# Kernel optimization log

Measured on AMD Instinct MI355X. Metric: run time of the kernel, lower is better.

The kernel has to match this reference:

```python
import jax, jax.numpy as jnp
import numpy as np

B, T, D = 4, 2048, 512
H, HS = 8, 64            # n_head, head_size
E, K = 8, 2              # num_experts, top_k
CAP = int(B * T * K / E * 1.0)  # expert capacity = 2048
EPS = 1e-5


def setup_inputs() -> dict:
    key = jax.random.key(0)
    ks = jax.random.split(key, 16)
    s = lambda k, shp, fan: jax.random.normal(k, shp, jnp.float32) * (fan ** -0.5)
    return {
        "x": jax.random.normal(ks[0], (B, T, D), jnp.float32),
        "ln1_g": jnp.ones((D,), jnp.float32), "ln1_b": jnp.zeros((D,), jnp.float32),
        "Wq": s(ks[1], (H, D, HS), D), "Wk": s(ks[2], (H, D, HS), D), "Wv": s(ks[3], (H, D, HS), D),
        "Wo": s(ks[4], (D, D), D), "bo": jnp.zeros((D,), jnp.float32),
        "ln2_g": jnp.ones((D,), jnp.float32), "ln2_b": jnp.zeros((D,), jnp.float32),
        "Wg": s(ks[5], (D, E), D), "bg": jnp.zeros((E,), jnp.float32),
        "Wn": s(ks[6], (D, E), D), "bn": jnp.zeros((E,), jnp.float32),
        "W1": s(ks[7], (E, D, 4 * D), D), "b1": jnp.zeros((E, 4 * D), jnp.float32),
        "W2": s(ks[8], (E, 4 * D, D), 4 * D), "b2": jnp.zeros((E, D), jnp.float32),
    }


def _ln(x, g, b):
    m = jnp.mean(x, -1, keepdims=True)
    v = jnp.var(x, -1, keepdims=True)
    return (x - m) * jax.lax.rsqrt(v + EPS) * g + b


def _attn(h, Wq, Wk, Wv, Wo, bo):
    q = jnp.einsum('btd,hde->bhte', h, Wq)
    k = jnp.einsum('btd,hde->bhte', h, Wk)
    v = jnp.einsum('btd,hde->bhte', h, Wv)
    # NOTE: source scales by C**-0.5 with C = n_embed (not head_size)
    wei = jnp.einsum('bhte,bhse->bhts', q, k) * (D ** -0.5)
    causal = jnp.tril(jnp.ones((T, T), bool))
    wei = jnp.where(causal, wei, -jnp.inf)
    wei = jax.nn.softmax(wei, axis=-1)
    out = jnp.einsum('bhts,bhse->bhte', wei, v)              # [B,H,T,HS]
    out = out.transpose(0, 2, 1, 3).reshape(B, T, D)          # concat heads
    return out @ Wo + bo


def _moe(h, Wg, bg, Wn, bn, W1, b1, W2, b2):
    logits = h @ Wg + bg
    noise_logits = h @ Wn + bn
    noise = jax.random.normal(jax.random.key(42), logits.shape, logits.dtype) * jax.nn.softplus(noise_logits)
    noisy = logits + noise
    vals, idx = jax.lax.top_k(noisy, K)                       # [B,T,K]
    # softmax over -inf-masked sparse logits == softmax over top-k values, scattered
    gates = (jax.nn.softmax(vals, -1)[..., None] * jax.nn.one_hot(idx, E, dtype=h.dtype)).sum(-2)  # [B,T,E]
    flat_x = h.reshape(-1, D)
    flat_g = gates.reshape(-1, E)
    flat_idx = idx.reshape(-1, K)
    N = flat_x.shape[0]
    mask = (flat_idx[None] == jnp.arange(E)[:, None, None]).any(-1)   # [E,N]
    rank = jnp.cumsum(mask, axis=1) - 1
    keep = mask & (rank < CAP)                                 # first CAP tokens per expert
    slot = jnp.where(keep, rank, CAP)
    tok = jnp.arange(N, dtype=jnp.int32)

    def build(s, kp):
        buf = jnp.zeros(CAP + 1, jnp.int32).at[s].set(tok)
        vb = jnp.zeros(CAP + 1, bool).at[s].set(kp)
        return buf[:CAP], vb[:CAP]

    idx_buf, valid = jax.vmap(build)(slot, keep)               # [E,CAP]
    xg = flat_x[idx_buf]                                       # [E,CAP,D]
    mid = jax.nn.relu(jnp.einsum('ecd,edf->ecf', xg, W1) + b1[:, None, :])
    out = jnp.einsum('ecf,efd->ecd', mid, W2) + b2[:, None, :]
    gate_sel = flat_g[idx_buf, jnp.arange(E)[:, None]]         # [E,CAP]
    w = out * (gate_sel * valid.astype(h.dtype))[..., None]
    upd = jnp.zeros_like(flat_x).at[idx_buf.reshape(-1)].add(w.reshape(-1, D))
    return upd.reshape(h.shape)


def reference(x, ln1_g, ln1_b, Wq, Wk, Wv, Wo, bo, ln2_g, ln2_b,
              Wg, bg, Wn, bn, W1, b1, W2, b2):
    x = x + _attn(_ln(x, ln1_g, ln1_b), Wq, Wk, Wv, Wo, bo)
    x = x + _moe(_ln(x, ln2_g, ln2_b), Wg, bg, Wn, bn, W1, b1, W2, b2)
    return x
```

## Files before the change

kernel.cpp:

```cpp
#include <hip/hip_runtime.h>
#include <math.h>

#define TSEQ 2048
#define DD   512
#define NH   8
#define HSZ  64
#define NE   8
#define NTOK 8192
#define CAPK 2048
#define FF   2048

typedef __bf16 bf16x8 __attribute__((ext_vector_type(8)));
typedef float  f32x4  __attribute__((ext_vector_type(4)));
typedef unsigned int u32;
typedef u32 u32x4 __attribute__((ext_vector_type(4)));

__device__ __forceinline__ void gload16(const void* g, void* l){
  __builtin_amdgcn_global_load_lds((const __attribute__((address_space(1))) u32*)g,
                                   (__attribute__((address_space(3))) u32*)l, 16, 0, 0);
}

__device__ __forceinline__ u32 pkbf(float a, float b){
  unsigned short ua = __builtin_bit_cast(unsigned short, (__bf16)a);
  unsigned short ub = __builtin_bit_cast(unsigned short, (__bf16)b);
  return (u32)ua | ((u32)ub << 16);
}

__device__ __forceinline__ unsigned rotl32(unsigned x, int r){ return (x<<r)|(x>>(32-r)); }

__device__ __forceinline__ void threefry2x32(unsigned c0, unsigned c1, unsigned &o0, unsigned &o1){
  const unsigned k0 = 0u, k1 = 42u;
  const unsigned k2 = k0 ^ k1 ^ 0x1BD11BDAu;
  unsigned x0 = c0 + k0, x1 = c1 + k1;
#define TFR(rot) { x0 += x1; x1 = rotl32(x1, rot); x1 ^= x0; }
  TFR(13) TFR(15) TFR(26) TFR(6)   x0 += k1; x1 += k2 + 1u;
  TFR(17) TFR(29) TFR(16) TFR(24)  x0 += k2; x1 += k0 + 2u;
  TFR(13) TFR(15) TFR(26) TFR(6)   x0 += k0; x1 += k1 + 3u;
  TFR(17) TFR(29) TFR(16) TFR(24)  x0 += k1; x1 += k2 + 4u;
  TFR(13) TFR(15) TFR(26) TFR(6)   x0 += k2; x1 += k0 + 5u;
#undef TFR
  o0 = x0; o1 = x1;
}

__device__ __forceinline__ float erfinv_f(float x){
  float w = -log1pf(-x*x);
  float p;
  if (w < 5.0f){
    w -= 2.5f;
    p = 2.81022636e-08f;
    p = fmaf(p,w, 3.43273939e-07f);
    p = fmaf(p,w,-3.5233877e-06f);
    p = fmaf(p,w,-4.39150654e-06f);
    p = fmaf(p,w, 0.00021858087f);
    p = fmaf(p,w,-0.00125372503f);
    p = fmaf(p,w,-0.00417768164f);
    p = fmaf(p,w, 0.246640727f);
    p = fmaf(p,w, 1.50140941f);
  } else {
    w = sqrtf(w) - 3.0f;
    p = -0.000200214257f;
    p = fmaf(p,w, 0.000100950558f);
    p = fmaf(p,w, 0.00134934322f);
    p = fmaf(p,w,-0.00367342844f);
    p = fmaf(p,w, 0.00573950773f);
    p = fmaf(p,w,-0.0076224613f);
    p = fmaf(p,w, 0.00943887047f);
    p = fmaf(p,w, 1.00167406f);
    p = fmaf(p,w, 2.83297682f);
  }
  return p * x;
}

__global__ __launch_bounds__(256) void ln_split(const float* __restrict__ x,
    const float* __restrict__ gw, const float* __restrict__ bw,
    __bf16* __restrict__ ohi, __bf16* __restrict__ olo)
{
  int row  = blockIdx.x*4 + threadIdx.y;
  int lane = threadIdx.x;
  const float* xr = x + (size_t)row*DD;
  float4 a = *(const float4*)(xr + lane*4);
  float4 c = *(const float4*)(xr + 256 + lane*4);
  float s  = a.x+a.y+a.z+a.w + c.x+c.y+c.z+c.w;
  float ss = a.x*a.x+a.y*a.y+a.z*a.z+a.w*a.w + c.x*c.x+c.y*c.y+c.z*c.z+c.w*c.w;
  #pragma unroll
  for (int off = 32; off; off >>= 1){ s += __shfl_xor(s, off); ss += __shfl_xor(ss, off); }
  float m   = s * (1.0f/DD);
  float var = ss * (1.0f/DD) - m*m;
  float r   = 1.0f / sqrtf(var + 1e-5f);
  float4 g1 = *(const float4*)(gw + lane*4);
  float4 b1 = *(const float4*)(bw + lane*4);
  float4 g2 = *(const float4*)(gw + 256 + lane*4);
  float4 b2 = *(const float4*)(bw + 256 + lane*4);
  float f1[4], f2[4];
  f1[0]=(a.x-m)*r*g1.x+b1.x; f1[1]=(a.y-m)*r*g1.y+b1.y; f1[2]=(a.z-m)*r*g1.z+b1.z; f1[3]=(a.w-m)*r*g1.w+b1.w;
  f2[0]=(c.x-m)*r*g2.x+b2.x; f2[1]=(c.y-m)*r*g2.y+b2.y; f2[2]=(c.z-m)*r*g2.z+b2.z; f2[3]=(c.w-m)*r*g2.w+b2.w;
  __bf16 h1v[4] __attribute__((aligned(8))), l1v[4] __attribute__((aligned(8)));
  __bf16 h2v[4] __attribute__((aligned(8))), l2v[4] __attribute__((aligned(8)));
  #pragma unroll
  for (int j = 0; j < 4; ++j){
    __bf16 hb = (__bf16)f1[j]; h1v[j]=hb; l1v[j]=(__bf16)(f1[j]-(float)hb);
    __bf16 hc = (__bf16)f2[j]; h2v[j]=hc; l2v[j]=(__bf16)(f2[j]-(float)hc);
  }
  size_t base = (size_t)row*DD + lane*4;
  *(uint2*)(ohi + base)       = *(const uint2*)h1v;
  *(uint2*)(olo + base)       = *(const uint2*)l1v;
  *(uint2*)(ohi + base + 256) = *(const uint2*)h2v;
  *(uint2*)(olo + base + 256) = *(const uint2*)l2v;
}

__global__ __launch_bounds__(256) void pack_qkv_split(const float* __restrict__ Wq,
    const float* __restrict__ Wk, const float* __restrict__ Wv,
    __bf16* __restrict__ dhi, __bf16* __restrict__ dlo)
{
  __shared__ float t[64][65];
  int z = blockIdx.y;
  int kt = blockIdx.x*64;
  int sel = z >> 3, hh = z & 7;
  const float* W = (sel==0 ? Wq : (sel==1 ? Wk : Wv)) + (size_t)hh*DD*HSZ;
  int tid = threadIdx.x;
  int r = tid>>2, c0 = (tid&3)*16;
  #pragma unroll
  for (int j = 0; j < 16; j += 4){
    float4 v = *(const float4*)&W[(size_t)(kt+r)*HSZ + c0 + j];
    t[r][c0+j]=v.x; t[r][c0+j+1]=v.y; t[r][c0+j+2]=v.z; t[r][c0+j+3]=v.w;
  }
  __syncthreads();
  __bf16 hb[16] __attribute__((aligned(32)));
  __bf16 lb[16] __attribute__((aligned(32)));
  #pragma unroll
  for (int j = 0; j < 16; ++j){
    float f = t[c0+j][r];
    __bf16 h = (__bf16)f; hb[j]=h; lb[j]=(__bf16)(f-(float)h);
  }
  size_t off = (size_t)(z*64 + r)*512 + kt + c0;
  *(uint4*)(dhi+off) = ((const uint4*)hb)[0]; *(uint4*)(dhi+off+8) = ((const uint4*)hb)[1];
  *(uint4*)(dlo+off) = ((const uint4*)lb)[0]; *(uint4*)(dlo+off+8) = ((const uint4*)lb)[1];
}

__global__ __launch_bounds__(256) void transp_split(const float* __restrict__ src,
    __bf16* __restrict__ dhi, __bf16* __restrict__ dlo, int Ms, int Ns)
{
  __shared__ float t[64][65];
  int nt = blockIdx.x*64, mt = blockIdx.y*64;
  int tid = threadIdx.x;
  int r = tid>>2, c0 = (tid&3)*16;
  #pragma unroll
  for (int j = 0; j < 16; j += 4){
    float4 v = *(const float4*)&src[(size_t)(mt+r)*Ns + nt + c0 + j];
    t[r][c0+j]=v.x; t[r][c0+j+1]=v.y; t[r][c0+j+2]=v.z; t[r][c0+j+3]=v.w;
  }
  __syncthreads();
  __bf16 hb[16] __attribute__((aligned(32)));
  __bf16 lb[16] __attribute__((aligned(32)));
  #pragma unroll
  for (int j = 0; j < 16; ++j){
    float f = t[c0+j][r];
    __bf16 h = (__bf16)f; hb[j]=h; lb[j]=(__bf16)(f-(float)h);
  }
  size_t off = (size_t)(nt + r)*Ms + mt + c0;
  *(uint4*)(dhi+off) = ((const uint4*)hb)[0]; *(uint4*)(dhi+off+8) = ((const uint4*)hb)[1];
  *(uint4*)(dlo+off) = ((const uint4*)lb)[0]; *(uint4*)(dlo+off+8) = ((const uint4*)lb)[1];
}

template<int BIAS, int RES>
__global__ __launch_bounds__(256) void gemm_mfma3(
    const __bf16* __restrict__ Ahi, const __bf16* __restrict__ Alo,
    const __bf16* __restrict__ Bhi, const __bf16* __restrict__ Blo,
    const float* __restrict__ bias, const float* __restrict__ res,
    float* __restrict__ C, int M, int N, int K)
{
  __shared__ __bf16 AsH[2][4096];
  __shared__ __bf16 AsL[2][4096];
  __shared__ __bf16 BsH[2][4096];
  __shared__ __bf16 BsL[2][4096];
  int m0 = blockIdx.y*128, n0 = blockIdx.x*128;
  int tid = threadIdx.x;
  int w = tid>>6, l = tid&63;
  int wm = w>>1, wn = w&1;
  int srow = w*32 + (l>>2);
  int skb  = (l&3)<<4;
  const char* agh = (const char*)(Ahi + (size_t)(m0+srow)*K) + skb;
  const char* agl = (const char*)(Alo + (size_t)(m0+srow)*K) + skb;
  const char* bgh = (const char*)(Bhi + (size_t)(n0+srow)*K) + skb;
  const char* bgl = (const char*)(Blo + (size_t)(n0+srow)*K) + skb;
  size_t r16 = (size_t)16*K*sizeof(__bf16);

  f32x4 acc[4][4] = {};
  int rl = l & 15, kh = l >> 4;
  const __bf16* abh = &AsH[0][(wm*64 + rl)*32 + kh*8];
  const __bf16* abl = &AsL[0][(wm*64 + rl)*32 + kh*8];
  const __bf16* bbh = &BsH[0][(wn*64 + rl)*32 + kh*8];
  const __bf16* bbl = &BsL[0][(wn*64 + rl)*32 + kh*8];

  auto STAGE = [&](int bb, int kt){
    size_t o = (size_t)kt*64;
    gload16(agh+o,     &AsH[bb][w*1024]);
    gload16(agh+o+r16, &AsH[bb][w*1024+512]);
    gload16(agl+o,     &AsL[bb][w*1024]);
    gload16(agl+o+r16, &AsL[bb][w*1024+512]);
    gload16(bgh+o,     &BsH[bb][w*1024]);
    gload16(bgh+o+r16, &BsH[bb][w*1024+512]);
    gload16(bgl+o,     &BsL[bb][w*1024]);
    gload16(bgl+o+r16, &BsL[bb][w*1024+512]);
  };

  int nkt = K >> 5;
  STAGE(0, 0);
  __syncthreads();
  for (int kt = 0; kt < nkt; ++kt){
    int bb = kt & 1;
    if (kt + 1 < nkt) STAGE(bb^1, kt+1);
    bf16x8 afh[4], afl[4], bfh[4], bfl[4];
    #pragma unroll
    for (int i = 0; i < 4; ++i){
      afh[i] = *(const bf16x8*)(abh + bb*4096 + i*512);
      afl[i] = *(const bf16x8*)(abl + bb*4096 + i*512);
      bfh[i] = *(const bf16x8*)(bbh + bb*4096 + i*512);
      bfl[i] = *(const bf16x8*)(bbl + bb*4096 + i*512);
    }
    #pragma unroll
    for (int fm = 0; fm < 4; ++fm)
      #pragma unroll
      for (int fn = 0; fn < 4; ++fn){
        acc[fm][fn] = __builtin_amdgcn_mfma_f32_16x16x32_bf16(afh[fm], bfl[fn], acc[fm][fn], 0, 0, 0);
        acc[fm][fn] = __builtin_amdgcn_mfma_f32_16x16x32_bf16(afl[fm], bfh[fn], acc[fm][fn], 0, 0, 0);
        acc[fm][fn] = __builtin_amdgcn_mfma_f32_16x16x32_bf16(afh[fm], bfh[fn], acc[fm][fn], 0, 0, 0);
      }
    __syncthreads();
  }

  int ccol = l & 15, cr = (l >> 4) * 4;
  #pragma unroll
  for (int fn = 0; fn < 4; ++fn){
    int n = n0 + wn*64 + fn*16 + ccol;
    float bv = BIAS ? bias[n] : 0.0f;
    #pragma unroll
    for (int fm = 0; fm < 4; ++fm){
      int mb = m0 + wm*64 + fm*16 + cr;
      #pragma unroll
      for (int r = 0; r < 4; ++r){
        float v = acc[fm][fn][r] + bv;
        if (RES) v += res[(size_t)(mb+r)*N + n];
        C[(size_t)(mb+r)*N + n] = v;
      }
    }
  }
}

template<int STORE_BF16, int RELU, int GATHER, int LOGN>
__global__ __launch_bounds__(256) void gemm_mfma(
    const __bf16* __restrict__ A, const __bf16* __restrict__ Bt,
    const float* __restrict__ bias, void* __restrict__ Cv,
    const int* __restrict__ idxb, int M, int N, int K)
{
  __shared__ __bf16 Asl[2][4096];
  __shared__ __bf16 Bsl[2][4096];
  int flat = blockIdx.x;
  int e = flat & 3;
  int tile = flat >> 2;
  int n0 = (tile & ((1<<LOGN)-1)) * 128;
  int m0 = (tile >> LOGN) * 128;
  const __bf16* Be = Bt + (size_t)e*N*K;
  const float*  be = bias + (size_t)e*N;
  int tid = threadIdx.x;
  int w = tid>>6, l = tid&63;
  int wm = w>>1, wn = w&1;
  int srow = w*32 + (l>>2);
  int skb  = (l&3)<<4;
  const char* ag;
  if (GATHER){
    int tok = idxb[e*CAPK + m0 + srow];
    ag = (const char*)(A + (size_t)tok*K) + skb;
  } else {
    ag = (const char*)(A + (size_t)e*M*K + (size_t)(m0 + srow)*K) + skb;
  }
  const char* bg = (const char*)(Be + (size_t)(n0 + srow)*K) + skb;
  size_t r16;
  if (GATHER){
    int tok2 = idxb[e*CAPK + m0 + srow + 16];
    r16 = (size_t)((const char*)(A + (size_t)tok2*K) + skb - ag);
  } else {
    r16 = (size_t)16*K*sizeof(__bf16);
  }

  f32x4 acc[4][4] = {};
  int rl = l & 15, kh = l >> 4;
  const __bf16* abase = &Asl[0][(wm*64 + rl)*32 + kh*8];
  const __bf16* bbase = &Bsl[0][(wn*64 + rl)*32 + kh*8];

  size_t br16 = (size_t)16*K*sizeof(__bf16);
  auto STAGE = [&](int bb, int kt){
    size_t o = (size_t)kt*64;
    gload16(ag+o,      &Asl[bb][w*1024]);
    gload16(ag+o+r16,  &Asl[bb][w*1024+512]);
    gload16(bg+o,      &Bsl[bb][w*1024]);
    gload16(bg+o+br16, &Bsl[bb][w*1024+512]);
  };

  int nkt = K >> 5;
  STAGE(0, 0);
  __syncthreads();
  for (int kt = 0; kt < nkt; ++kt){
    int bb = kt & 1;
    if (kt + 1 < nkt) STAGE(bb^1, kt+1);
    bf16x8 af[4], bf[4];
    #pragma unroll
    for (int i = 0; i < 4; ++i){
      af[i] = *(const bf16x8*)(abase + bb*4096 + i*512);
      bf[i] = *(const bf16x8*)(bbase + bb*4096 + i*512);
    }
    #pragma unroll
    for (int fm = 0; fm < 4; ++fm)
      #pragma unroll
      for (int fn = 0; fn < 4; ++fn)
        acc[fm][fn] = __builtin_amdgcn_mfma_f32_16x16x32_bf16(af[fm], bf[fn], acc[fm][fn], 0, 0, 0);
    __syncthreads();
  }

  int ccol = l & 15, cr = (l >> 4) * 4;
  char* Ce = (char*)Cv + (size_t)e*M*N*(STORE_BF16 ? 2 : 4);
  #pragma unroll
  for (int fn = 0; fn < 4; ++fn){
    int n = n0 + wn*64 + fn*16 + ccol;
    float bv = be[n];
    #pragma unroll
    for (int fm = 0; fm < 4; ++fm){
      int mb = m0 + wm*64 + fm*16 + cr;
      #pragma unroll
      for (int r = 0; r < 4; ++r){
        float v = acc[fm][fn][r] + bv;
        if (RELU) v = fmaxf(v, 0.f);
        if (STORE_BF16) ((__bf16*)Ce)[(size_t)(mb+r)*N + n] = (__bf16)v;
        else            ((float*)Ce)[(size_t)(mb+r)*N + n] = v;
      }
    }
  }
}

__global__ __launch_bounds__(256) void transp_conv(const float* __restrict__ src,
    __bf16* __restrict__ dst, int Ms, int Ns)
{
  __shared__ __bf16 t[64][72];
  int e = blockIdx.z;
  const float* s = src + (size_t)e*Ms*Ns;
  __bf16* d = dst + (size_t)e*Ms*Ns;
  int mt = blockIdx.y*64, nt = blockIdx.x*64;
  int tid = threadIdx.x;
  int r = tid>>2, c0 = (tid&3)*16;
  #pragma unroll
  for (int j = 0; j < 16; j += 4){
    float4 v = *(const float4*)&s[(size_t)(mt+r)*Ns + nt + c0 + j];
    t[r][c0+j]   = (__bf16)v.x; t[r][c0+j+1] = (__bf16)v.y;
    t[r][c0+j+2] = (__bf16)v.z; t[r][c0+j+3] = (__bf16)v.w;
  }
  __syncthreads();
  __bf16 tmp[16] __attribute__((aligned(32)));
  #pragma unroll
  for (int j = 0; j < 16; ++j) tmp[j] = t[c0+j][r];
  uint4* dp = (uint4*)&d[(size_t)(nt+r)*Ms + mt + c0];
  dp[0] = ((const uint4*)tmp)[0];
  dp[1] = ((const uint4*)tmp)[1];
}

__global__ __launch_bounds__(256) void convert_kv(const float* __restrict__ qkv,
    __bf16* __restrict__ khi, __bf16* __restrict__ klo,
    __bf16* __restrict__ vthi, __bf16* __restrict__ vtlo)
{
  int t0 = blockIdx.x*64;
  int bh = blockIdx.y;
  int b = bh >> 3, h = bh & 7;
  int tid = threadIdx.x;
  {
    int r = tid >> 2, e0 = (tid & 3) * 16;
    const float* src = qkv + ((size_t)(b*TSEQ + t0 + r))*1536 + 512 + h*64 + e0;
    __bf16 hi[16] __attribute__((aligned(16)));
    __bf16 lo[16] __attribute__((aligned(16)));
    #pragma unroll
    for (int j = 0; j < 16; j += 4){
      float4 v = *(const float4*)(src + j);
      float f[4] = {v.x, v.y, v.z, v.w};
      #pragma unroll
      for (int q = 0; q < 4; ++q){
        __bf16 hb = (__bf16)f[q];
        hi[j+q] = hb; lo[j+q] = (__bf16)(f[q] - (float)hb);
      }
    }
    size_t off = ((size_t)(bh*TSEQ + t0 + r))*64 + e0;
    *(uint4*)(khi + off)     = ((const uint4*)hi)[0];
    *(uint4*)(khi + off + 8) = ((const uint4*)hi)[1];
    *(uint4*)(klo + off)     = ((const uint4*)lo)[0];
    *(uint4*)(klo + off + 8) = ((const uint4*)lo)[1];
  }
  {
    int key0 = (tid & 15) * 4, e0 = (tid >> 4) * 4;
    float4 v[4];
    #pragma unroll
    for (int j = 0; j < 4; ++j)
      v[j] = *(const float4*)(qkv + ((size_t)(b*TSEQ + t0 + key0 + j))*1536 + 1024 + h*64 + e0);
    float col[4][4];
    col[0][0]=v[0].x; col[0][1]=v[1].x; col[0][2]=v[2].x; col[0][3]=v[3].x;
    col[1][0]=v[0].y; col[1][1]=v[1].y; col[1][2]=v[2].y; col[1][3]=v[3].y;
    col[2][0]=v[0].z; col[2][1]=v[1].z; col[2][2]=v[2].z; col[2][3]=v[3].z;
    col[3][0]=v[0].w; col[3][1]=v[1].w; col[3][2]=v[2].w; col[3][3]=v[3].w;
    #pragma unroll
    for (int kk = 0; kk < 4; ++kk){
      __bf16 hi[4] __attribute__((aligned(8)));
      __bf16 lo[4] __attribute__((aligned(8)));
      #pragma unroll
      for (int j = 0; j < 4; ++j){
        __bf16 hb = (__bf16)col[kk][j];
        hi[j] = hb; lo[j] = (__bf16)(col[kk][j] - (float)hb);
      }
      size_t off = ((size_t)(bh*64 + e0 + kk))*TSEQ + t0 + key0;
      *(uint2*)(vthi + off) = *(const uint2*)hi;
      *(uint2*)(vtlo + off) = *(const uint2*)lo;
    }
  }
}

__global__ __launch_bounds__(512) void attn_mfma(const float* __restrict__ qkv,
    const __bf16* __restrict__ khi_g, const __bf16* __restrict__ klo_g,
    const __bf16* __restrict__ vthi_g, const __bf16* __restrict__ vtlo_g,
    __bf16* __restrict__ ahi, __bf16* __restrict__ alo)
{
  __shared__ __align__(16) char ldsbuf[65536];
  int bh = blockIdx.x;
  int qtA = blockIdx.y, qtB = 15 - qtA;
  int b = bh >> 3, h = bh & 7;
  int tid = threadIdx.x;
  int w = tid >> 6, l = tid & 63;
  int g = l >> 4, r = l & 15;
  int sA = r + 32*(g & 1);
  int sB = sA + 16;
  int ghalf = g >> 1;
  const float qsc = 0.04419417382415922f * 1.4426950408889634f;

  int qb[2]; qb[0] = qtA*128 + w*16; qb[1] = qtB*128 + (7-w)*16;
  int kdiag[2]; kdiag[0] = qb[0] >> 6; kdiag[1] = qb[1] >> 6;

  bf16x8 qhi[2][2], qlo[2][2];
  #pragma unroll
  for (int qf = 0; qf < 2; ++qf)
    #pragma unroll
    for (int ks = 0; ks < 2; ++ks){
      const float* src = qkv + ((size_t)(b*TSEQ + qb[qf] + r))*1536 + h*64 + ks*32 + g*8;
      float4 v0 = *(const float4*)src;
      float4 v1 = *(const float4*)(src + 4);
      float f[8] = {v0.x,v0.y,v0.z,v0.w,v1.x,v1.y,v1.z,v1.w};
      bf16x8 hi, lo;
      #pragma unroll
      for (int i = 0; i < 8; ++i){
        float fs = f[i] * qsc;
        __bf16 hb = (__bf16)fs;
        hi[i] = hb; lo[i] = (__bf16)(fs - (float)hb);
      }
      qhi[qf][ks] = hi; qlo[qf][ks] = lo;
    }

  f32x4 ot[4][2] = {};
  float m_r[2] = {-INFINITY, -INFINITY};
  float l_r[2] = {0.f, 0.f};

  int nkt = 2*qtB + 2;
  size_t kbase = (size_t)bh*TSEQ*64;
  size_t vbase = (size_t)bh*64*TSEQ;

  auto STAGE = [&](int buf, int kt){
    int row = tid >> 3, cc = tid & 7;
    int sw = (cc ^ (row & 7)) * 8;
    char* d = ldsbuf + buf*32768 + (w << 10);
    gload16(khi_g  + kbase + (size_t)(kt*64 + row)*64 + sw, d);
    gload16(klo_g  + kbase + (size_t)(kt*64 + row)*64 + sw, d + 8192);
    gload16(vthi_g + vbase + (size_t)row*TSEQ + kt*64 + sw,  d + 16384);
    gload16(vtlo_g + vbase + (size_t)row*TSEQ + kt*64 + sw,  d + 24576);
  };

  STAGE(0, 0);
  __syncthreads();

  for (int kt = 0; kt < nkt; ++kt){
    int buf = kt & 1;
    if (kt + 1 < nkt) STAGE(buf ^ 1, kt + 1);

    bool act[2];
    act[0] = (kt <= kdiag[0]);
    act[1] = (kt <= kdiag[1]);

    const char* K0 = ldsbuf + buf*32768;
    const char* K1 = K0 + 8192;
    const char* V0 = K0 + 16384;
    const char* V1 = K0 + 24576;

    f32x4 s[4][2] = {};
    #pragma unroll
    for (int kf = 0; kf < 4; ++kf){
      int rowk = kf*16 + r;
      int rsw = (rowk & 7) << 4;
      #pragma unroll
      for (int ks = 0; ks < 2; ++ks){
        int off = rowk*128 + ((((ks*4 + g) << 4)) ^ rsw);
        bf16x8 khf = *(const bf16x8*)(K0 + off);
        bf16x8 klf = *(const bf16x8*)(K1 + off);
        #pragma unroll
        for (int qf = 0; qf < 2; ++qf){
          if (act[qf]){
            s[kf][qf] = __builtin_amdgcn_mfma_f32_16x16x32_bf16(khf, qlo[qf][ks], s[kf][qf], 0,0,0);
            s[kf][qf] = __builtin_amdgcn_mfma_f32_16x16x32_bf16(klf, qhi[qf][ks], s[kf][qf], 0,0,0);
            s[kf][qf] = __builtin_amdgcn_mfma_f32_16x16x32_bf16(khf, qhi[qf][ks], s[kf][qf], 0,0,0);
          }
        }
      }
    }

    u32 phi[4][2][2], plo[4][2][2];
    #pragma unroll
    for (int qf = 0; qf < 2; ++qf){
      if (act[qf]){
        int q = qb[qf] + r;
        float p[4][4];
        float mx = -INFINITY;
        if (kt == kdiag[qf]){
          #pragma unroll
          for (int kf = 0; kf < 4; ++kf)
            #pragma unroll
            for (int e = 0; e < 4; ++e){
              int key = kt*64 + kf*16 + g*4 + e;
              float sv = (key <= q) ? s[kf][qf][e] : -INFINITY;
              p[kf][e] = sv;
              mx = fmaxf(mx, sv);
            }
        } else {
          #pragma unroll
          for (int kf = 0; kf < 4; ++kf)
            #pragma unroll
            for (int e = 0; e < 4; ++e){
              float sv = s[kf][qf][e];
              p[kf][e] = sv;
              mx = fmaxf(mx, sv);
            }
        }
        mx = fmaxf(mx, __shfl_xor(mx, 16));
        mx = fmaxf(mx, __shfl_xor(mx, 32));
        if (__any(mx > m_r[qf])){
          float mn = fmaxf(m_r[qf], mx);
          float fj = exp2f(m_r[qf] - mn);
          m_r[qf] = mn;
          l_r[qf] *= fj;
          #pragma unroll
          for (int ef = 0; ef < 4; ++ef)
            #pragma unroll
            for (int e = 0; e < 4; ++e)
              ot[ef][qf][e] *= fj;
        }
        float ts = 0.f;
        #pragma unroll
        for (int kf = 0; kf < 4; ++kf)
          #pragma unroll
          for (int e = 0; e < 4; ++e){
            float pv = exp2f(p[kf][e] - m_r[qf]);
            p[kf][e] = pv; ts += pv;
          }
        ts += __shfl_xor(ts, 16); ts += __shfl_xor(ts, 32);
        l_r[qf] += ts;
        #pragma unroll
        for (int kf = 0; kf < 4; ++kf){
          __bf16 h0=(__bf16)p[kf][0], h1=(__bf16)p[kf][1], h2=(__bf16)p[kf][2], h3=(__bf16)p[kf][3];
          phi[kf][qf][0] = pkbf(p[kf][0], p[kf][1]);
          phi[kf][qf][1] = pkbf(p[kf][2], p[kf][3]);
          plo[kf][qf][0] = pkbf(p[kf][0]-(float)h0, p[kf][1]-(float)h1);
          plo[kf][qf][1] = pkbf(p[kf][2]-(float)h2, p[kf][3]-(float)h3);
        }
      }
    }

    #pragma unroll
    for (int ks = 0; ks < 2; ++ks){
      u32x4 pbh[2], pbl[2];
      #pragma unroll
      for (int qf = 0; qf < 2; ++qf){
        if (act[qf]){
          #pragma unroll
          for (int p2 = 0; p2 < 2; ++p2){
            u32 hA0 = (u32)__shfl((int)phi[2*ks  ][qf][p2], sA);
            u32 hA1 = (u32)__shfl((int)phi[2*ks+1][qf][p2], sA);
            u32 hB0 = (u32)__shfl((int)phi[2*ks  ][qf][p2], sB);
            u32 hB1 = (u32)__shfl((int)phi[2*ks+1][qf][p2], sB);
            pbh[qf][p2]   = ghalf ? hA1 : hA0;
            pbh[qf][2+p2] = ghalf ? hB1 : hB0;
            u32 lA0 = (u32)__shfl((int)plo[2*ks  ][qf][p2], sA);
            u32 lA1 = (u32)__shfl((int)plo[2*ks+1][qf][p2], sA);
            u32 lB0 = (u32)__shfl((int)plo[2*ks  ][qf][p2], sB);
            u32 lB1 = (u32)__shfl((int)plo[2*ks+1][qf][p2], sB);
            pbl[qf][p2]   = ghalf ? lA1 : lA0;
            pbl[qf][2+p2] = ghalf ? lB1 : lB0;
          }
        }
      }
      #pragma unroll
      for (int ef = 0; ef < 4; ++ef){
        int rowv = ef*16 + r;
        int off = rowv*128 + ((((ks*4 + g) << 4)) ^ ((rowv & 7) << 4));
        bf16x8 vhf = *(const bf16x8*)(V0 + off);
        bf16x8 vlf = *(const bf16x8*)(V1 + off);
        #pragma unroll
        for (int qf = 0; qf < 2; ++qf){
          if (act[qf]){
            bf16x8 ph = __builtin_bit_cast(bf16x8, pbh[qf]);
            bf16x8 pl = __builtin_bit_cast(bf16x8, pbl[qf]);
            ot[ef][qf] = __builtin_amdgcn_mfma_f32_16x16x32_bf16(vhf, pl, ot[ef][qf], 0,0,0);
            ot[ef][qf] = __builtin_amdgcn_mfma_f32_16x16x32_bf16(vlf, ph, ot[ef][qf], 0,0,0);
            ot[ef][qf] = __builtin_amdgcn_mfma_f32_16x16x32_bf16(vhf, ph, ot[ef][qf], 0,0,0);
          }
        }
      }
    }
    __syncthreads();
  }

  float* Osh = (float*)ldsbuf;
  #pragma unroll
  for (int qf = 0; qf < 2; ++qf){
    float inv = 1.0f / l_r[qf];
    int qloc = (qf ? (7-w) : w)*16 + r;
    #pragma unroll
    for (int ef = 0; ef < 4; ++ef)
      #pragma unroll
      for (int e = 0; e < 4; ++e)
        Osh[qloc*68 + ef*16 + g*4 + e] = ot[ef][qf][e] * inv;
    __syncthreads();
    {
      int qt = qf ? qtB : qtA;
      int q = tid >> 2, e0 = (tid & 3)*16;
      const float* srow = Osh + q*68 + e0;
      size_t base = ((size_t)(b*TSEQ + qt*128 + q))*DD + h*64 + e0;
      #pragma unroll
      for (int j = 0; j < 4; ++j){
        float4 v = *(const float4*)(srow + j*4);
        float f[4] = {v.x, v.y, v.z, v.w};
        __bf16 hb[4] __attribute__((aligned(8)));
        __bf16 lb[4] __attribute__((aligned(8)));
        #pragma unroll
        for (int q2 = 0; q2 < 4; ++q2){
          __bf16 h2b = (__bf16)f[q2];
          hb[q2] = h2b; lb[q2] = (__bf16)(f[q2] - (float)h2b);
        }
        *(uint2*)(ahi + base + j*4) = *(const uint2*)hb;
        *(uint2*)(alo + base + j*4) = *(const uint2*)lb;
      }
    }
    __syncthreads();
  }
}

__global__ __launch_bounds__(256) void routerln_kernel(const float* __restrict__ x1,
    const float* __restrict__ gw, const float* __restrict__ bw,
    const float* __restrict__ Wg, const float* __restrict__ bg,
    const float* __restrict__ Wn, const float* __restrict__ bn,
    __bf16* __restrict__ h2b,
    int* __restrict__ idx0, int* __restrict__ idx1,
    float* __restrict__ g0, float* __restrict__ g1)
{
  int wid = threadIdx.x >> 6, lane = threadIdx.x & 63;
  int tok = blockIdx.x*4 + wid;
  const float* xr = x1 + (size_t)tok*DD;
  float4 a = *(const float4*)(xr + lane*4);
  float4 c = *(const float4*)(xr + 256 + lane*4);
  float s  = a.x+a.y+a.z+a.w + c.x+c.y+c.z+c.w;
  float ss = a.x*a.x+a.y*a.y+a.z*a.z+a.w*a.w + c.x*c.x+c.y*c.y+c.z*c.z+c.w*c.w;
  #pragma unroll
  for (int off = 32; off; off >>= 1){ s += __shfl_xor(s, off); ss += __shfl_xor(ss, off); }
  float m   = s * (1.0f/DD);
  float var = ss * (1.0f/DD) - m*m;
  float rr  = 1.0f / sqrtf(var + 1e-5f);
  float4 g1v = *(const float4*)(gw + lane*4);
  float4 b1v = *(const float4*)(bw + lane*4);
  float4 g2v = *(const float4*)(gw + 256 + lane*4);
  float4 b2v = *(const float4*)(bw + 256 + lane*4);
  float f1[4], f2[4];
  f1[0]=(a.x-m)*rr*g1v.x+b1v.x; f1[1]=(a.y-m)*rr*g1v.y+b1v.y; f1[2]=(a.z-m)*rr*g1v.z+b1v.z; f1[3]=(a.w-m)*rr*g1v.w+b1v.w;
  f2[0]=(c.x-m)*rr*g2v.x+b2v.x; f2[1]=(c.y-m)*rr*g2v.y+b2v.y; f2[2]=(c.z-m)*rr*g2v.z+b2v.z; f2[3]=(c.w-m)*rr*g2v.w+b2v.w;
  {
    __bf16 h1v[4] __attribute__((aligned(8)));
    __bf16 h2v[4] __attribute__((aligned(8)));
    #pragma unroll
    for (int j = 0; j < 4; ++j){ h1v[j] = (__bf16)f1[j]; h2v[j] = (__bf16)f2[j]; }
    size_t base = (size_t)tok*DD + lane*4;
    *(uint2*)(h2b + base)       = *(const uint2*)h1v;
    *(uint2*)(h2b + base + 256) = *(const uint2*)h2v;
  }
  float ag[8] = {0,0,0,0,0,0,0,0}, an[8] = {0,0,0,0,0,0,0,0};
  int d1 = lane*4, d2 = 256 + lane*4;
  #pragma unroll
  for (int j = 0; j < 4; ++j){
    const float* wg1 = Wg + (size_t)(d1+j)*8;
    const float* wn1 = Wn + (size_t)(d1+j)*8;
    const float* wg2 = Wg + (size_t)(d2+j)*8;
    const float* wn2 = Wn + (size_t)(d2+j)*8;
    #pragma unroll
    for (int e = 0; e < 8; ++e){
      ag[e] = fmaf(f1[j], wg1[e], ag[e]); an[e] = fmaf(f1[j], wn1[e], an[e]);
      ag[e] = fmaf(f2[j], wg2[e], ag[e]); an[e] = fmaf(f2[j], wn2[e], an[e]);
    }
  }
  #pragma unroll
  for (int off = 32; off; off >>= 1){
    #pragma unroll
    for (int e = 0; e < 8; ++e){ ag[e] += __shfl_xor(ag[e], off); an[e] += __shfl_xor(an[e], off); }
  }
  __shared__ float ns[4][8];
  if (lane < 8){
    int e = lane;
    float lg = ag[e] + bg[e];
    float nl = an[e] + bn[e];
    float sp = fmaxf(nl, 0.f) + log1pf(expf(-fabsf(nl)));
    unsigned i = (unsigned)(tok*8 + e);
    unsigned r0b, r1b;
    threefry2x32(0u, i, r0b, r1b);
    unsigned bits = r0b ^ r1b;
    float f = __uint_as_float((bits >> 9) | 0x3f800000u) - 1.0f;
    float u = fmaf(f, 2.0f, -0.99999994f);
    u = fmaxf(u, -0.99999994f);
    float z = 1.41421356f * erfinv_f(u);
    ns[wid][e] = lg + z*sp;
  }
  __syncthreads();
  if (lane == 0){
    float v0 = -INFINITY; int i0 = 0;
    #pragma unroll
    for (int e = 0; e < 8; ++e){ float v = ns[wid][e]; if (v > v0){ v0 = v; i0 = e; } }
    float v1 = -INFINITY; int i1 = 0;
    #pragma unroll
    for (int e = 0; e < 8; ++e){ if (e != i0){ float v = ns[wid][e]; if (v > v1){ v1 = v; i1 = e; } } }
    float dexp = expf(v1 - v0);
    float ssum = 1.0f + dexp;
    idx0[tok] = i0; idx1[tok] = i1;
    g0[tok] = 1.0f/ssum; g1[tok] = dexp/ssum;
  }
}

__global__ __launch_bounds__(256) void route_scan(const int* __restrict__ idx0,
    const int* __restrict__ idx1, int* __restrict__ idx_buf, int* __restrict__ tok_slot)
{
  int e = blockIdx.x, tid = threadIdx.x;
  for (int i = tid; i < CAPK; i += 256) idx_buf[e*CAPK + i] = 0;
  __syncthreads();
  int base = tid * 32;
  int cnt = 0;
  for (int j = 0; j < 32; ++j){ int t = base + j; cnt += (idx0[t]==e || idx1[t]==e) ? 1 : 0; }
  __shared__ int ps[256];
  ps[tid] = cnt; __syncthreads();
  for (int off = 1; off < 256; off <<= 1){
    int add = (tid >= off) ? ps[tid - off] : 0;
    __syncthreads();
    ps[tid] += add;
    __syncthreads();
  }
  int slot = ps[tid] - cnt;
  for (int j = 0; j < 32; ++j){
    int t = base + j;
    int k = (idx0[t]==e) ? 0 : ((idx1[t]==e) ? 1 : -1);
    if (k >= 0){
      if (slot < CAPK){ idx_buf[e*CAPK + slot] = t; tok_slot[t*2 + k] = slot; }
      else            { tok_slot[t*2 + k] = -1; }
      slot++;
    }
  }
}

__global__ __launch_bounds__(128) void combine_kernel(const float* __restrict__ x1,
    const __bf16* __restrict__ eout, const int* __restrict__ idx0, const int* __restrict__ idx1,
    const float* __restrict__ g0, const float* __restrict__ g1,
    const int* __restrict__ tok_slot, float* __restrict__ outp)
{
  int n = blockIdx.x, t = threadIdx.x;
  float4 acc = *(const float4*)(x1 + (size_t)n*DD + t*4);
  #pragma unroll
  for (int k = 0; k < 2; ++k){
    int s = tok_slot[n*2 + k];
    if (s >= 0){
      int e  = (k==0) ? idx0[n] : idx1[n];
      float g = (k==0) ? g0[n] : g1[n];
      __bf16 vb[4] __attribute__((aligned(8)));
      *(uint2*)vb = *(const uint2*)(eout + ((size_t)(e*CAPK + s))*DD + t*4);
      acc.x = fmaf(g, (float)vb[0], acc.x); acc.y = fmaf(g, (float)vb[1], acc.y);
      acc.z = fmaf(g, (float)vb[2], acc.z); acc.w = fmaf(g, (float)vb[3], acc.w);
    }
  }
  *(float4*)(outp + (size_t)n*DD + t*4) = acc;
}

extern "C" void kernel_launch(void* const* d_in, const int* in_sizes, int n_in,
                              void* d_out, int out_size, void* d_ws, size_t ws_size,
                              hipStream_t stream)
{
  const float* x    = (const float*)d_in[0];
  const float* ln1g = (const float*)d_in[1];
  const float* ln1b = (const float*)d_in[2];
  const float* Wq   = (const float*)d_in[3];
  const float* Wk   = (const float*)d_in[4];
  const float* Wv   = (const float*)d_in[5];
  const float* Wo   = (const float*)d_in[6];
  const float* bo   = (const float*)d_in[7];
  const float* ln2g = (const float*)d_in[8];
  const float* ln2b = (const float*)d_in[9];
  const float* Wg   = (const float*)d_in[10];
  const float* bg   = (const float*)d_in[11];
  const float* Wn   = (const float*)d_in[12];
  const float* bn   = (const float*)d_in[13];
  const float* W1   = (const float*)d_in[14];
  const float* b1   = (const float*)d_in[15];
  const float* W2   = (const float*)d_in[16];
  const float* b2   = (const float*)d_in[17];
  float* out = (float*)d_out;
  char* ws = (char*)d_ws;
  const size_t MB = 1u << 20;

  __bf16* h1hi   = (__bf16*)(ws);
  __bf16* h1lo   = (__bf16*)(ws + 8*MB);
  __bf16* attnhi = (__bf16*)(ws);
  __bf16* attnlo = (__bf16*)(ws + 8*MB);
  __bf16* h2b    = (__bf16*)(ws);
  float*  qkv    = (float*)(ws + 16*MB);
  __bf16* W1T    = (__bf16*)(ws + 16*MB);
  __bf16* W2T    = (__bf16*)(ws + 32*MB);
  float*  x1     = (float*)(ws + 64*MB);
  __bf16* Khi    = (__bf16*)(ws + 80*MB);
  __bf16* Klo    = (__bf16*)(ws + 88*MB);
  __bf16* Vthi   = (__bf16*)(ws + 96*MB);
  __bf16* Vtlo   = (__bf16*)(ws + 104*MB);
  __bf16* Bqh    = (__bf16*)(ws + 80*MB);
  __bf16* Bql    = (__bf16*)(ws + 82*MB);
  __bf16* eoutb  = (__bf16*)(ws + 80*MB);
  __bf16* mid    = (__bf16*)(ws + 112*MB);
  __bf16* WoTh   = (__bf16*)(ws + 144*MB);
  __bf16* WoTl   = (__bf16*)(ws + 144*MB + 512*1024);
  char*   smallp = ws + 145*MB;
  int*   idx0     = (int*)smallp;
  int*   idx1     = idx0 + NTOK;
  float* g0       = (float*)(idx1 + NTOK);
  float* g1       = g0 + NTOK;
  int*   tok_slot = (int*)(g1 + NTOK);
  int*   idx_buf  = tok_slot + NTOK*2;

  ln_split<<<dim3(NTOK/4), dim3(64,4), 0, stream>>>(x, ln1g, ln1b, h1hi, h1lo);
  pack_qkv_split<<<dim3(8,24), 256, 0, stream>>>(Wq, Wk, Wv, Bqh, Bql);
  transp_split<<<dim3(8,8), 256, 0, stream>>>(Wo, WoTh, WoTl, DD, DD);
  gemm_mfma3<0,0><<<dim3(12,64), 256, 0, stream>>>(h1hi, h1lo, Bqh, Bql, nullptr, nullptr, qkv, NTOK, 1536, DD);
  convert_kv<<<dim3(TSEQ/64, 32), 256, 0, stream>>>(qkv, Khi, Klo, Vthi, Vtlo);
  attn_mfma<<<dim3(32, 8), 512, 0, stream>>>(qkv, Khi, Klo, Vthi, Vtlo, attnhi, attnlo);
  gemm_mfma3<1,1><<<dim3(4,64), 256, 0, stream>>>(attnhi, attnlo, WoTh, WoTl, bo, x, x1, NTOK, DD, DD);
  routerln_kernel<<<dim3(NTOK/4), 256, 0, stream>>>(x1, ln2g, ln2b, Wg, bg, Wn, bn,
      h2b, idx0, idx1, g0, g1);
  transp_conv<<<dim3(32,8,NE), 256, 0, stream>>>(W1, W1T, DD, FF);
  transp_conv<<<dim3(8,32,NE), 256, 0, stream>>>(W2, W2T, FF, DD);
  route_scan<<<dim3(NE), 256, 0, stream>>>(idx0, idx1, idx_buf, tok_slot);
  for (int gg = 0; gg < 2; ++gg){
    gemm_mfma<1,1,1,4><<<dim3(4*16*16), 256, 0, stream>>>(
        h2b, W1T + (size_t)gg*4*DD*FF, b1 + (size_t)gg*4*FF,
        mid, idx_buf + (size_t)gg*4*CAPK, CAPK, FF, DD);
    gemm_mfma<1,0,0,2><<<dim3(4*4*16), 256, 0, stream>>>(
        mid, W2T + (size_t)gg*4*FF*DD, b2 + (size_t)gg*4*DD,
        eoutb + (size_t)gg*4*CAPK*DD, nullptr, CAPK, DD, FF);
  }
  combine_kernel<<<dim3(NTOK), 128, 0, stream>>>(x1, eoutb, idx0, idx1, g0, g1, tok_slot, out);
}
```

Before: 433.6 us.

## Use 16x16x16 MFMA for PV to drop shuffles; merge expert GEMMs into single launches

```diff
diff --git a/kernel.cpp b/kernel.cpp
--- a/kernel.cpp
+++ b/kernel.cpp
@@ -13,7 +13,8 @@
 typedef __bf16 bf16x8 __attribute__((ext_vector_type(8)));
 typedef float  f32x4  __attribute__((ext_vector_type(4)));
 typedef unsigned int u32;
-typedef u32 u32x4 __attribute__((ext_vector_type(4)));
+typedef u32 u32x2 __attribute__((ext_vector_type(2)));
+typedef short s16x4 __attribute__((ext_vector_type(4)));
 
 __device__ __forceinline__ void gload16(const void* g, void* l){
   __builtin_amdgcn_global_load_lds((const __attribute__((address_space(1))) u32*)g,
@@ -24,6 +25,11 @@
   unsigned short ua = __builtin_bit_cast(unsigned short, (__bf16)a);
   unsigned short ub = __builtin_bit_cast(unsigned short, (__bf16)b);
   return (u32)ua | ((u32)ub << 16);
+}
+
+__device__ __forceinline__ s16x4 mk4(u32 a, u32 b){
+  u32x2 t; t[0] = a; t[1] = b;
+  return __builtin_bit_cast(s16x4, t);
 }
 
 __device__ __forceinline__ unsigned rotl32(unsigned x, int r){ return (x<<r)|(x>>(32-r)); }
@@ -247,7 +253,7 @@
   }
 }
 
-template<int STORE_BF16, int RELU, int GATHER, int LOGN>
+template<int STORE_BF16, int RELU, int GATHER, int LOGN, int EBITS>
 __global__ __launch_bounds__(256) void gemm_mfma(
     const __bf16* __restrict__ A, const __bf16* __restrict__ Bt,
     const float* __restrict__ bias, void* __restrict__ Cv,
@@ -256,8 +262,8 @@
   __shared__ __bf16 Asl[2][4096];
   __shared__ __bf16 Bsl[2][4096];
   int flat = blockIdx.x;
-  int e = flat & 3;
-  int tile = flat >> 2;
+  int e = flat & ((1<<EBITS)-1);
+  int tile = flat >> EBITS;
   int n0 = (tile & ((1<<LOGN)-1)) * 128;
   int m0 = (tile >> LOGN) * 128;
   const __bf16* Be = Bt + (size_t)e*N*K;
@@ -430,9 +436,6 @@
   int tid = threadIdx.x;
   int w = tid >> 6, l = tid & 63;
   int g = l >> 4, r = l & 15;
-  int sA = r + 32*(g & 1);
-  int sB = sA + 16;
-  int ghalf = g >> 1;
   const float qsc = 0.04419417382415922f * 1.4426950408889634f;
 
   int qb[2]; qb[0] = qtA*128 + w*16; qb[1] = qtB*128 + (7-w)*16;
@@ -574,42 +577,21 @@
     }
 
     #pragma unroll
-    for (int ks = 0; ks < 2; ++ks){
-      u32x4 pbh[2], pbl[2];
-      #pragma unroll
-      for (int qf = 0; qf < 2; ++qf){
-        if (act[qf]){
-          #pragma unroll
-          for (int p2 = 0; p2 < 2; ++p2){
-            u32 hA0 = (u32)__shfl((int)phi[2*ks  ][qf][p2], sA);
-            u32 hA1 = (u32)__shfl((int)phi[2*ks+1][qf][p2], sA);
-            u32 hB0 = (u32)__shfl((int)phi[2*ks  ][qf][p2], sB);
-            u32 hB1 = (u32)__shfl((int)phi[2*ks+1][qf][p2], sB);
-            pbh[qf][p2]   = ghalf ? hA1 : hA0;
-            pbh[qf][2+p2] = ghalf ? hB1 : hB0;
-            u32 lA0 = (u32)__shfl((int)plo[2*ks  ][qf][p2], sA);
-            u32 lA1 = (u32)__shfl((int)plo[2*ks+1][qf][p2], sA);
-            u32 lB0 = (u32)__shfl((int)plo[2*ks  ][qf][p2], sB);
-            u32 lB1 = (u32)__shfl((int)plo[2*ks+1][qf][p2], sB);
-            pbl[qf][p2]   = ghalf ? lA1 : lA0;
-            pbl[qf][2+p2] = ghalf ? lB1 : lB0;
-          }
-        }
-      }
+    for (int kf = 0; kf < 4; ++kf){
       #pragma unroll
       for (int ef = 0; ef < 4; ++ef){
         int rowv = ef*16 + r;
-        int off = rowv*128 + ((((ks*4 + g) << 4)) ^ ((rowv & 7) << 4));
-        bf16x8 vhf = *(const bf16x8*)(V0 + off);
-        bf16x8 vlf = *(const bf16x8*)(V1 + off);
+        int off = rowv*128 + ((((2*kf + (g>>1)) ^ (rowv & 7)) << 4)) + (g&1)*8;
+        s16x4 vh = *(const s16x4*)(V0 + off);
+        s16x4 vl = *(const s16x4*)(V1 + off);
         #pragma unroll
         for (int qf = 0; qf < 2; ++qf){
           if (act[qf]){
-            bf16x8 ph = __builtin_bit_cast(bf16x8, pbh[qf]);
-            bf16x8 pl = __builtin_bit_cast(bf16x8, pbl[qf]);
-            ot[ef][qf] = __builtin_amdgcn_mfma_f32_16x16x32_bf16(vhf, pl, ot[ef][qf], 0,0,0);
-            ot[ef][qf] = __builtin_amdgcn_mfma_f32_16x16x32_bf16(vlf, ph, ot[ef][qf], 0,0,0);
-            ot[ef][qf] = __builtin_amdgcn_mfma_f32_16x16x32_bf16(vhf, ph, ot[ef][qf], 0,0,0);
+            s16x4 ph = mk4(phi[kf][qf][0], phi[kf][qf][1]);
+            s16x4 pl = mk4(plo[kf][qf][0], plo[kf][qf][1]);
+            ot[ef][qf] = __builtin_amdgcn_mfma_f32_16x16x16bf16_1k(vh, pl, ot[ef][qf], 0,0,0);
+            ot[ef][qf] = __builtin_amdgcn_mfma_f32_16x16x16bf16_1k(vl, ph, ot[ef][qf], 0,0,0);
+            ot[ef][qf] = __builtin_amdgcn_mfma_f32_16x16x16bf16_1k(vh, ph, ot[ef][qf], 0,0,0);
           }
         }
       }
@@ -823,6 +805,7 @@
   float*  qkv    = (float*)(ws + 16*MB);
   __bf16* W1T    = (__bf16*)(ws + 16*MB);
   __bf16* W2T    = (__bf16*)(ws + 32*MB);
+  __bf16* eoutb  = (__bf16*)(ws + 48*MB);
   float*  x1     = (float*)(ws + 64*MB);
   __bf16* Khi    = (__bf16*)(ws + 80*MB);
   __bf16* Klo    = (__bf16*)(ws + 88*MB);
@@ -830,8 +813,7 @@
   __bf16* Vtlo   = (__bf16*)(ws + 104*MB);
   __bf16* Bqh    = (__bf16*)(ws + 80*MB);
   __bf16* Bql    = (__bf16*)(ws + 82*MB);
-  __bf16* eoutb  = (__bf16*)(ws + 80*MB);
-  __bf16* mid    = (__bf16*)(ws + 112*MB);
+  __bf16* mid    = (__bf16*)(ws + 80*MB);
   __bf16* WoTh   = (__bf16*)(ws + 144*MB);
   __bf16* WoTl   = (__bf16*)(ws + 144*MB + 512*1024);
   char*   smallp = ws + 145*MB;
@@ -854,13 +836,9 @@
   transp_conv<<<dim3(32,8,NE), 256, 0, stream>>>(W1, W1T, DD, FF);
   transp_conv<<<dim3(8,32,NE), 256, 0, stream>>>(W2, W2T, FF, DD);
   route_scan<<<dim3(NE), 256, 0, stream>>>(idx0, idx1, idx_buf, tok_slot);
-  for (int gg = 0; gg < 2; ++gg){
-    gemm_mfma<1,1,1,4><<<dim3(4*16*16), 256, 0, stream>>>(
-        h2b, W1T + (size_t)gg*4*DD*FF, b1 + (size_t)gg*4*FF,
-        mid, idx_buf + (size_t)gg*4*CAPK, CAPK, FF, DD);
-    gemm_mfma<1,0,0,2><<<dim3(4*4*16), 256, 0, stream>>>(
-        mid, W2T + (size_t)gg*4*FF*DD, b2 + (size_t)gg*4*DD,
-        eoutb + (size_t)gg*4*CAPK*DD, nullptr, CAPK, DD, FF);
-  }
+  gemm_mfma<1,1,1,4,3><<<dim3(8*16*16), 256, 0, stream>>>(
+      h2b, W1T, b1, mid, idx_buf, CAPK, FF, DD);
+  gemm_mfma<1,0,0,2,3><<<dim3(8*16*4), 256, 0, stream>>>(
+      mid, W2T, b2, eoutb, nullptr, CAPK, DD, FF);
   combine_kernel<<<dim3(NTOK), 128, 0, stream>>>(x1, eoutb, idx0, idx1, g0, g1, tok_slot, out);
 }
```

Measured after the change: 384.8 us. 1.13x faster.
